# Kernel tuning notes

Measured on AMD Instinct MI355X. Metric: run time of the kernel, lower is better.

Reference implementation:

```python
import jax, jax.numpy as jnp
import numpy as np

B, N = 1, 1024
C_S, C_Z, N_HEAD, C_HEAD = 384, 128, 16, 24
HC = N_HEAD * C_HEAD


def _ln(x, eps=1e-5):
    m = jnp.mean(x, axis=-1, keepdims=True)
    v = jnp.var(x, axis=-1, keepdims=True)
    return (x - m) / jnp.sqrt(v + eps)


def setup_inputs() -> dict:
    key = jax.random.key(0)
    ks = jax.random.split(key, 24)
    w = lambda k, shp: (jax.random.normal(k, shp, jnp.float32) * 0.02)
    return {
        "a_i": jax.random.normal(ks[0], (B, N, C_S), jnp.float32),
        "s_i": jax.random.normal(ks[1], (B, N, C_S), jnp.float32),
        "z_ij": jax.random.normal(ks[2], (B, N, N, C_Z), jnp.float32),
        # AdaLN params
        "adaln_lns_w": jnp.ones((C_S,), jnp.float32),      # layer_norm_s weight (no bias)
        "adaln_ws": w(ks[3], (C_S, C_S)),                   # linear_s weight
        "adaln_bs": jnp.zeros((C_S,), jnp.float32),         # linear_s bias
        "adaln_wns": w(ks[4], (C_S, C_S)),                  # linear_no_bias_s
        # attention projections
        "wq": w(ks[5], (C_S, HC)),
        "bq": jnp.zeros((HC,), jnp.float32),
        "wk": w(ks[6], (C_S, HC)),
        "wv": w(ks[7], (C_S, HC)),
        # pair bias
        "lnb_w": jnp.ones((C_Z,), jnp.float32),
        "lnb_b": jnp.zeros((C_Z,), jnp.float32),
        "wb": w(ks[8], (C_Z, N_HEAD)),
        # gate + output
        "wg": w(ks[9], (C_S, HC)),
        "wo": w(ks[10], (HC, C_S)),
        # final conditioning gate (bias init -2.0 per module)
        "ws": w(ks[11], (C_S, C_S)),
        "bs": jnp.full((C_S,), -2.0, jnp.float32),
    }


def reference(a_i, s_i, z_ij, adaln_lns_w, adaln_ws, adaln_bs, adaln_wns,
              wq, bq, wk, wv, lnb_w, lnb_b, wb, wg, wo, ws, bs):
    b, n, _ = a_i.shape
    H, D = N_HEAD, C_HEAD
    # AdaLN: a <- sigmoid(Lin(s)) * LN(a) + Lin_nb(s)
    a = _ln(a_i)
    s = _ln(s_i) * adaln_lns_w
    a = jax.nn.sigmoid(s @ adaln_ws + adaln_bs) * a + s @ adaln_wns
    # QKV projections -> [b, i, h, d]
    q = (a @ wq + bq).reshape(b, n, H, D)
    k = (a @ wk).reshape(b, n, H, D)
    v = (a @ wv).reshape(b, n, H, D)
    # pair bias [b, h, i, j]
    bias = jnp.einsum('bijc,ch->bhij', _ln(z_ij) * lnb_w + lnb_b, wb)
    # gate [b, i, h, d]
    g = jax.nn.sigmoid(a @ wg).reshape(b, n, H, D)
    logits = jnp.einsum('bihd,bjhd->bhij', q, k) / jnp.sqrt(jnp.float32(D)) + bias
    A = jax.nn.softmax(logits, axis=-1)
    o = jnp.einsum('bhij,bjhd->bihd', A, v) * g
    o = o.reshape(b, n, H * D) @ wo
    # final gate uses raw s_i
    return jax.nn.sigmoid(s_i @ ws + bs) * o
```

## Files before the change

kernel.cpp:

```cpp
#include <hip/hip_runtime.h>
#include <hip/hip_bf16.h>
#include <math.h>

#define N_SEQ 1024
#define CS 384
#define CZ 128
#define NH 16
#define CH 24

typedef float  floatx4 __attribute__((ext_vector_type(4)));
typedef short  shortx8 __attribute__((ext_vector_type(8)));
typedef unsigned int uintx4 __attribute__((ext_vector_type(4)));

__device__ __forceinline__ unsigned short f2bf(float f){
  union { float fv; unsigned u; } c; c.fv = f;
  unsigned u = c.u;
  return (unsigned short)((u + 0x7fffu + ((u >> 16) & 1u)) >> 16);
}
__device__ __forceinline__ float bf2f(unsigned short s){
  union { unsigned u; float fv; } c; c.u = ((unsigned)s) << 16; return c.fv;
}
__device__ __forceinline__ float bf_lo(unsigned u){
  union { unsigned uu; float f; } c; c.uu = u << 16; return c.f;
}
__device__ __forceinline__ float bf_hi(unsigned u){
  union { unsigned uu; float f; } c; c.uu = u & 0xffff0000u; return c.f;
}
__device__ __forceinline__ float sigmoidf_(float x){ return 1.f / (1.f + __expf(-x)); }

__global__ __launch_bounds__(128) void ln_kernel(
    const float* __restrict__ a_i, const float* __restrict__ s_i,
    const float* __restrict__ lns_w,
    float* __restrict__ a_ln, float* __restrict__ s_ln)
{
  int i = blockIdx.x;
  int t = threadIdx.x;
  float av[3], sv[3];
  float sa = 0.f, qa = 0.f, ss = 0.f, qs = 0.f;
  #pragma unroll
  for (int e = 0; e < 3; ++e){
    int c = t + 128*e;
    float a = a_i[(size_t)i*CS + c];
    float s = s_i[(size_t)i*CS + c];
    av[e] = a; sv[e] = s;
    sa += a; qa += a*a; ss += s; qs += s*s;
  }
  #pragma unroll
  for (int off = 1; off < 64; off <<= 1){
    sa += __shfl_xor(sa, off);
    qa += __shfl_xor(qa, off);
    ss += __shfl_xor(ss, off);
    qs += __shfl_xor(qs, off);
  }
  __shared__ float red[2][4];
  if ((t & 63) == 0){
    int w = t >> 6;
    red[w][0] = sa; red[w][1] = qa; red[w][2] = ss; red[w][3] = qs;
  }
  __syncthreads();
  const float inv = 1.f / CS;
  float Sa = red[0][0] + red[1][0];
  float Qa = red[0][1] + red[1][1];
  float Ss = red[0][2] + red[1][2];
  float Qs = red[0][3] + red[1][3];
  float ma = Sa*inv, va = Qa*inv - ma*ma, ra = rsqrtf(va + 1e-5f);
  float ms = Ss*inv, vs = Qs*inv - ms*ms, rs = rsqrtf(vs + 1e-5f);
  #pragma unroll
  for (int e = 0; e < 3; ++e){
    int c = t + 128*e;
    a_ln[(size_t)i*CS + c] = (av[e] - ma) * ra;
    s_ln[(size_t)i*CS + c] = (sv[e] - ms) * rs * lns_w[c];
  }
}

__global__ __launch_bounds__(384) void gemm_kernel(
    const float* __restrict__ X, const float* __restrict__ W1,
    const float* __restrict__ B1, const float* __restrict__ W2,
    const float* __restrict__ extra,
    float* __restrict__ OUT1, float* __restrict__ OUT2, int mode)
{
  int r0 = blockIdx.x * 4;
  int t  = threadIdx.x;
  int ct = t % 96;
  int rg = t / 96;
  int c0 = ct * 4;
  __shared__ float xl[4][CS];
  #pragma unroll
  for (int rr = 0; rr < 4; ++rr)
    xl[rr][t] = X[(size_t)(r0+rr)*CS + t];
  __syncthreads();
  float acc1[4] = {0.f,0.f,0.f,0.f};
  float acc2[4] = {0.f,0.f,0.f,0.f};
  if (mode <= 2){
    for (int k = 0; k < CS; k += 4){
      floatx4 s4 = *(const floatx4*)&xl[rg][k];
      #pragma unroll
      for (int kk = 0; kk < 4; ++kk){
        floatx4 w1 = *(const floatx4*)&W1[(size_t)(k+kk)*CS + c0];
        floatx4 w2 = *(const floatx4*)&W2[(size_t)(k+kk)*CS + c0];
        #pragma unroll
        for (int cc = 0; cc < 4; ++cc){
          acc1[cc] += s4[kk] * w1[cc];
          acc2[cc] += s4[kk] * w2[cc];
        }
      }
    }
  } else {
    for (int k = 0; k < CS; k += 4){
      floatx4 s4 = *(const floatx4*)&xl[rg][k];
      #pragma unroll
      for (int kk = 0; kk < 4; ++kk){
        floatx4 w1 = *(const floatx4*)&W1[(size_t)(k+kk)*CS + c0];
        #pragma unroll
        for (int cc = 0; cc < 4; ++cc)
          acc1[cc] += s4[kk] * w1[cc];
      }
    }
  }
  int r = r0 + rg;
  size_t ob = (size_t)r * CS + c0;
  if (mode == 0){
    #pragma unroll
    for (int cc = 0; cc < 4; ++cc)
      OUT1[ob+cc] = sigmoidf_(acc1[cc] + B1[c0+cc]) * extra[ob+cc] + acc2[cc];
  } else if (mode == 1){
    #pragma unroll
    for (int cc = 0; cc < 4; ++cc){
      OUT1[ob+cc] = acc1[cc] + B1[c0+cc];
      OUT2[ob+cc] = acc2[cc];
    }
  } else if (mode == 2){
    #pragma unroll
    for (int cc = 0; cc < 4; ++cc){
      OUT1[ob+cc] = acc1[cc];
      OUT2[ob+cc] = sigmoidf_(acc2[cc]);
    }
  } else if (mode == 3){
    #pragma unroll
    for (int cc = 0; cc < 4; ++cc)
      OUT1[ob+cc] = acc1[cc];
  } else {
    #pragma unroll
    for (int cc = 0; cc < 4; ++cc)
      OUT1[ob+cc] = sigmoidf_(acc1[cc] + B1[c0+cc]) * extra[ob+cc];
  }
}

__global__ __launch_bounds__(256) void bias_kernel(
    const float* __restrict__ z, const float* __restrict__ lnb_w,
    const float* __restrict__ lnb_b, const float* __restrict__ wb,
    unsigned short* __restrict__ bias)
{
  int i    = blockIdx.x >> 4;
  int j0   = (blockIdx.x & 15) * 64;
  int wave = threadIdx.x >> 6;
  int lane = threadIdx.x & 63;
  int m    = lane & 15;
  int q    = lane >> 4;
  int jbase = j0 + wave * 16;

  shortx8 bfrag[4];
  float sumw = 0.f, sumb = 0.f;
  #pragma unroll
  for (int s = 0; s < 4; ++s){
    #pragma unroll
    for (int jj = 0; jj < 8; ++jj){
      int c = q*8 + jj + 32*s;
      float lw = lnb_w[c];
      float lb = lnb_b[c];
      float w  = wb[c*NH + m];
      bfrag[s][jj] = (short)f2bf(lw * w);
      sumw += lw * w;
      sumb += lb * w;
    }
  }
  sumw += __shfl_xor(sumw, 16); sumw += __shfl_xor(sumw, 32);
  sumb += __shfl_xor(sumb, 16); sumb += __shfl_xor(sumb, 32);

  const float* zrow = z + ((size_t)i * N_SEQ + (size_t)(jbase + m)) * CZ;
  floatx4 acc = {0.f, 0.f, 0.f, 0.f};
  float sum = 0.f, sq = 0.f;
  #pragma unroll
  for (int s = 0; s < 4; ++s){
    floatx4 z0 = *(const floatx4*)(zrow + q*8 + 32*s);
    floatx4 z1 = *(const floatx4*)(zrow + q*8 + 32*s + 4);
    shortx8 af;
    #pragma unroll
    for (int e = 0; e < 4; ++e){
      sum += z0[e]; sq += z0[e]*z0[e];
      sum += z1[e]; sq += z1[e]*z1[e];
      af[e]   = (short)f2bf(z0[e]);
      af[e+4] = (short)f2bf(z1[e]);
    }
    acc = __builtin_amdgcn_mfma_f32_16x16x32_bf16(af, bfrag[s], acc, 0, 0, 0);
  }
  sum += __shfl_xor(sum, 16); sum += __shfl_xor(sum, 32);
  sq  += __shfl_xor(sq , 16); sq  += __shfl_xor(sq , 32);
  float mean = sum * (1.f/CZ);
  float var  = sq  * (1.f/CZ) - mean*mean;
  float rstd = rsqrtf(var + 1e-5f);

  __shared__ float ob[NH][65];
  #pragma unroll
  for (int r = 0; r < 4; ++r){
    int row = q*4 + r;
    float mr = __shfl(mean, row);
    float rr = __shfl(rstd, row);
    ob[m][wave*16 + row] = rr * (acc[r] - mr * sumw) + sumb;
  }
  __syncthreads();
  size_t base = (size_t)i * N_SEQ + j0;
  #pragma unroll
  for (int rep = 0; rep < 4; ++rep){
    int idx = threadIdx.x + rep*256;
    int hh = idx >> 6;
    int jj = idx & 63;
    bias[(size_t)hh * ((size_t)N_SEQ*N_SEQ) + base + jj] = f2bf(ob[hh][jj]);
  }
}

#define TJ 128
#define KROW 20
__global__ __launch_bounds__(256) void attn_kernel(
    const float* __restrict__ qq, const float* __restrict__ kk,
    const float* __restrict__ vv, const float* __restrict__ gg,
    const unsigned short* __restrict__ bias, float* __restrict__ att)
{
  int h  = blockIdx.x & 15;
  int i0 = (blockIdx.x >> 4) * 16;
  int il = threadIdx.x & 15;
  int jg = threadIdx.x >> 4;

  __shared__ unsigned int smem[TJ*KROW*2];

  float qr[24];
  {
    const float* qs = qq + (size_t)(i0+il)*CS + h*CH;
    #pragma unroll
    for (int e = 0; e < 6; ++e){
      floatx4 t4 = *(const floatx4*)(qs + 4*e);
      qr[4*e] = t4[0]; qr[4*e+1] = t4[1]; qr[4*e+2] = t4[2]; qr[4*e+3] = t4[3];
    }
  }
  const float scale = 0.20412414523193154f;
  float lrun = 0.f;
  float o[24];
  #pragma unroll
  for (int d = 0; d < 24; ++d) o[d] = 0.f;

  for (int jt = 0; jt < 8; ++jt){
    __syncthreads();
    {
      int row  = threadIdx.x >> 1;
      int half = threadIdx.x & 1;
      const float* ks = kk + (size_t)(jt*TJ + row)*CS + h*CH + half*12;
      const float* vs = vv + (size_t)(jt*TJ + row)*CS + h*CH + half*12;
      unsigned int* kd = smem + row*KROW + half*6;
      unsigned int* vd = smem + TJ*KROW + row*KROW + half*6;
      #pragma unroll
      for (int e = 0; e < 6; ++e){
        kd[e] = (unsigned)f2bf(ks[2*e]) | ((unsigned)f2bf(ks[2*e+1]) << 16);
        vd[e] = (unsigned)f2bf(vs[2*e]) | ((unsigned)f2bf(vs[2*e+1]) << 16);
      }
    }
    __syncthreads();
    const unsigned short* bptr = bias + (size_t)h*((size_t)N_SEQ*N_SEQ)
                               + (size_t)(i0+il)*N_SEQ + jt*TJ;
    #pragma unroll
    for (int tt = 0; tt < 8; ++tt){
      int jl = jg + 16*tt;
      uintx4 k0 = *(const uintx4*)&smem[jl*KROW];
      uintx4 k1 = *(const uintx4*)&smem[jl*KROW + 4];
      uintx4 k2 = *(const uintx4*)&smem[jl*KROW + 8];
      float dot = 0.f;
      #pragma unroll
      for (int e = 0; e < 4; ++e){
        dot += bf_lo(k0[e])*qr[2*e]      + bf_hi(k0[e])*qr[2*e+1];
        dot += bf_lo(k1[e])*qr[8+2*e]    + bf_hi(k1[e])*qr[8+2*e+1];
        dot += bf_lo(k2[e])*qr[16+2*e]   + bf_hi(k2[e])*qr[16+2*e+1];
      }
      float p = __expf(dot * scale + bf2f(bptr[jl]));
      lrun += p;
      uintx4 v0 = *(const uintx4*)&smem[TJ*KROW + jl*KROW];
      uintx4 v1 = *(const uintx4*)&smem[TJ*KROW + jl*KROW + 4];
      uintx4 v2 = *(const uintx4*)&smem[TJ*KROW + jl*KROW + 8];
      #pragma unroll
      for (int e = 0; e < 4; ++e){
        o[2*e]      += p * bf_lo(v0[e]);  o[2*e+1]    += p * bf_hi(v0[e]);
        o[8+2*e]    += p * bf_lo(v1[e]);  o[8+2*e+1]  += p * bf_hi(v1[e]);
        o[16+2*e]   += p * bf_lo(v2[e]);  o[16+2*e+1] += p * bf_hi(v2[e]);
      }
    }
  }
  __syncthreads();
  #pragma unroll
  for (int d = 0; d < 24; ++d){
    o[d] += __shfl_xor(o[d], 16);
    o[d] += __shfl_xor(o[d], 32);
  }
  lrun += __shfl_xor(lrun, 16);
  lrun += __shfl_xor(lrun, 32);
  float* mgf = (float*)smem;
  int lane = threadIdx.x & 63;
  int w    = threadIdx.x >> 6;
  if (lane < 16){
    float* slot = mgf + (w*16 + lane)*25;
    slot[0] = lrun;
    #pragma unroll
    for (int d = 0; d < 24; ++d) slot[1+d] = o[d];
  }
  __syncthreads();
  if (threadIdx.x < 16){
    int ii = threadIdx.x;
    float L = 0.f, O[24];
    #pragma unroll
    for (int d = 0; d < 24; ++d) O[d] = 0.f;
    for (int w2 = 0; w2 < 4; ++w2){
      const float* slot = mgf + (w2*16 + ii)*25;
      L += slot[0];
      #pragma unroll
      for (int d = 0; d < 24; ++d) O[d] += slot[1+d];
    }
    const float* gs = gg + (size_t)(i0+ii)*CS + h*CH;
    float* os = att + (size_t)(i0+ii)*CS + h*CH;
    float invL = 1.f / L;
    #pragma unroll
    for (int d = 0; d < 24; ++d) os[d] = O[d] * invL * gs[d];
  }
}

extern "C" void kernel_launch(void* const* d_in, const int* in_sizes, int n_in,
                              void* d_out, int out_size, void* d_ws, size_t ws_size,
                              hipStream_t stream) {
  const float* a_i     = (const float*)d_in[0];
  const float* s_i     = (const float*)d_in[1];
  const float* z_ij    = (const float*)d_in[2];
  const float* lns_w   = (const float*)d_in[3];
  const float* ada_ws  = (const float*)d_in[4];
  const float* ada_bs  = (const float*)d_in[5];
  const float* ada_wns = (const float*)d_in[6];
  const float* wq      = (const float*)d_in[7];
  const float* bq      = (const float*)d_in[8];
  const float* wk      = (const float*)d_in[9];
  const float* wv      = (const float*)d_in[10];
  const float* lnb_w   = (const float*)d_in[11];
  const float* lnb_b   = (const float*)d_in[12];
  const float* wb      = (const float*)d_in[13];
  const float* wg      = (const float*)d_in[14];
  const float* wo      = (const float*)d_in[15];
  const float* wsm     = (const float*)d_in[16];
  const float* bsv     = (const float*)d_in[17];

  const size_t RC = (size_t)N_SEQ * CS;
  float* wsf  = (float*)d_ws;
  float* s_ln = wsf;
  float* a_ln = wsf + RC;
  float* a    = wsf + 2*RC;
  float* qv   = wsf + 3*RC;
  float* kv   = wsf + 4*RC;
  float* vvp  = wsf + 5*RC;
  float* gv   = wsf + 6*RC;
  float* attb = wsf + 7*RC;
  float* tmp  = wsf + 8*RC;
  unsigned short* biasw = (unsigned short*)(wsf + 9*RC);

  ln_kernel<<<N_SEQ, 128, 0, stream>>>(a_i, s_i, lns_w, a_ln, s_ln);
  gemm_kernel<<<N_SEQ/4, 384, 0, stream>>>(s_ln, ada_ws, ada_bs, ada_wns, a_ln, a, nullptr, 0);
  gemm_kernel<<<N_SEQ/4, 384, 0, stream>>>(a, wq, bq, wk, nullptr, qv, kv, 1);
  gemm_kernel<<<N_SEQ/4, 384, 0, stream>>>(a, wv, nullptr, wg, nullptr, vvp, gv, 2);
  bias_kernel<<<N_SEQ*16, 256, 0, stream>>>(z_ij, lnb_w, lnb_b, wb, biasw);
  attn_kernel<<<N_SEQ, 256, 0, stream>>>(qv, kv, vvp, gv, biasw, attb);
  gemm_kernel<<<N_SEQ/4, 384, 0, stream>>>(attb, wo, nullptr, nullptr, nullptr, tmp, nullptr, 3);
  gemm_kernel<<<N_SEQ/4, 384, 0, stream>>>(s_i, wsm, bsv, nullptr, tmp, (float*)d_out, nullptr, 4);
}
```

Baseline: 1.171 ms.

## Overlap pair-bias computation with LN and projection GEMMs via horizontal kernel fusion

The standalone bias kernel is split into chunks of 3072, 6656 and 6656 work units. These run as extra blocks inside the LN, AdaLN and QKVG GEMM kernels, so the memory-bound z_ij streaming overlaps with the small latency-bound GEMMs. The Q/K/V/G projections are merged into one kernel that reads the activations once, and the output projection is fused with the final sigmoid gate. This removes launches and intermediate buffers, but mixes block types with different launch bounds and shared-memory use in the same grid.

```diff
diff --git a/kernel.cpp b/kernel.cpp
--- a/kernel.cpp
+++ b/kernel.cpp
@@ -7,6 +7,7 @@
 #define CZ 128
 #define NH 16
 #define CH 24
+#define HC 384
 
 typedef float  floatx4 __attribute__((ext_vector_type(4)));
 typedef short  shortx8 __attribute__((ext_vector_type(8)));
@@ -28,20 +29,106 @@
 }
 __device__ __forceinline__ float sigmoidf_(float x){ return 1.f / (1.f + __expf(-x)); }
 
-__global__ __launch_bounds__(128) void ln_kernel(
+__device__ __forceinline__ void bias_unit(int u, int tid, int nthr,
+    const float* __restrict__ z, const float* __restrict__ lnb_w,
+    const float* __restrict__ lnb_b, const float* __restrict__ wb,
+    unsigned short* __restrict__ bias, float (*ob)[65])
+{
+  int i    = u >> 4;
+  int j0   = (u & 15) * 64;
+  int wave = tid >> 6;
+  int lane = tid & 63;
+
+  if (wave < 4){
+    int m = lane & 15;
+    int q = lane >> 4;
+    int jbase = j0 + wave * 16;
+
+    shortx8 bfrag[4];
+    float sumw = 0.f, sumb = 0.f;
+    #pragma unroll
+    for (int s = 0; s < 4; ++s){
+      #pragma unroll
+      for (int jj = 0; jj < 8; ++jj){
+        int c = q*8 + jj + 32*s;
+        float lw = lnb_w[c];
+        float lb = lnb_b[c];
+        float w  = wb[c*NH + m];
+        bfrag[s][jj] = (short)f2bf(lw * w);
+        sumw += lw * w;
+        sumb += lb * w;
+      }
+    }
+    sumw += __shfl_xor(sumw, 16); sumw += __shfl_xor(sumw, 32);
+    sumb += __shfl_xor(sumb, 16); sumb += __shfl_xor(sumb, 32);
+
+    const float* zrow = z + ((size_t)i * N_SEQ + (size_t)(jbase + m)) * CZ;
+    floatx4 acc = {0.f, 0.f, 0.f, 0.f};
+    float sum = 0.f, sq = 0.f;
+    #pragma unroll
+    for (int s = 0; s < 4; ++s){
+      floatx4 z0 = *(const floatx4*)(zrow + q*8 + 32*s);
+      floatx4 z1 = *(const floatx4*)(zrow + q*8 + 32*s + 4);
+      shortx8 af;
+      #pragma unroll
+      for (int e = 0; e < 4; ++e){
+        sum += z0[e]; sq += z0[e]*z0[e];
+        sum += z1[e]; sq += z1[e]*z1[e];
+        af[e]   = (short)f2bf(z0[e]);
+        af[e+4] = (short)f2bf(z1[e]);
+      }
+      acc = __builtin_amdgcn_mfma_f32_16x16x32_bf16(af, bfrag[s], acc, 0, 0, 0);
+    }
+    sum += __shfl_xor(sum, 16); sum += __shfl_xor(sum, 32);
+    sq  += __shfl_xor(sq , 16); sq  += __shfl_xor(sq , 32);
+    float mean = sum * (1.f/CZ);
+    float var  = sq  * (1.f/CZ) - mean*mean;
+    float rstd = rsqrtf(var + 1e-5f);
+
+    #pragma unroll
+    for (int r = 0; r < 4; ++r){
+      int row = q*4 + r;
+      float mr = __shfl(mean, row);
+      float rr = __shfl(rstd, row);
+      ob[m][wave*16 + row] = rr * (acc[r] - mr * sumw) + sumb;
+    }
+  }
+  __syncthreads();
+  size_t base = (size_t)i * N_SEQ + j0;
+  for (int idx = tid; idx < NH*64; idx += nthr){
+    int hh = idx >> 6;
+    int jj = idx & 63;
+    bias[(size_t)hh * ((size_t)N_SEQ*N_SEQ) + base + jj] = f2bf(ob[hh][jj]);
+  }
+}
+
+#define LN_BLOCKS 512
+#define NB1 3072
+__global__ __launch_bounds__(256) void ln_bias_kernel(
     const float* __restrict__ a_i, const float* __restrict__ s_i,
     const float* __restrict__ lns_w,
-    float* __restrict__ a_ln, float* __restrict__ s_ln)
-{
-  int i = blockIdx.x;
-  int t = threadIdx.x;
+    float* __restrict__ a_ln, float* __restrict__ s_ln,
+    const float* __restrict__ z, const float* __restrict__ lnb_w,
+    const float* __restrict__ lnb_b, const float* __restrict__ wb,
+    unsigned short* __restrict__ biasw)
+{
+  __shared__ float ob[NH][65];
+  if (blockIdx.x >= LN_BLOCKS){
+    bias_unit(blockIdx.x - LN_BLOCKS, threadIdx.x, 256, z, lnb_w, lnb_b, wb, biasw, ob);
+    return;
+  }
+  float* red = &ob[0][0];
+  int t    = threadIdx.x;
+  int half = t >> 7;
+  int tl   = t & 127;
+  int row  = blockIdx.x*2 + half;
   float av[3], sv[3];
   float sa = 0.f, qa = 0.f, ss = 0.f, qs = 0.f;
   #pragma unroll
   for (int e = 0; e < 3; ++e){
-    int c = t + 128*e;
-    float a = a_i[(size_t)i*CS + c];
-    float s = s_i[(size_t)i*CS + c];
+    int c = tl + 128*e;
+    float a = a_i[(size_t)row*CS + c];
+    float s = s_i[(size_t)row*CS + c];
     av[e] = a; sv[e] = s;
     sa += a; qa += a*a; ss += s; qs += s*s;
   }
@@ -52,170 +139,127 @@
     ss += __shfl_xor(ss, off);
     qs += __shfl_xor(qs, off);
   }
-  __shared__ float red[2][4];
   if ((t & 63) == 0){
     int w = t >> 6;
-    red[w][0] = sa; red[w][1] = qa; red[w][2] = ss; red[w][3] = qs;
+    red[w*4+0] = sa; red[w*4+1] = qa; red[w*4+2] = ss; red[w*4+3] = qs;
   }
   __syncthreads();
   const float inv = 1.f / CS;
-  float Sa = red[0][0] + red[1][0];
-  float Qa = red[0][1] + red[1][1];
-  float Ss = red[0][2] + red[1][2];
-  float Qs = red[0][3] + red[1][3];
+  int wb0 = half*2;
+  float Sa = red[wb0*4+0] + red[(wb0+1)*4+0];
+  float Qa = red[wb0*4+1] + red[(wb0+1)*4+1];
+  float Ss = red[wb0*4+2] + red[(wb0+1)*4+2];
+  float Qs = red[wb0*4+3] + red[(wb0+1)*4+3];
   float ma = Sa*inv, va = Qa*inv - ma*ma, ra = rsqrtf(va + 1e-5f);
   float ms = Ss*inv, vs = Qs*inv - ms*ms, rs = rsqrtf(vs + 1e-5f);
   #pragma unroll
   for (int e = 0; e < 3; ++e){
-    int c = t + 128*e;
-    a_ln[(size_t)i*CS + c] = (av[e] - ma) * ra;
-    s_ln[(size_t)i*CS + c] = (sv[e] - ms) * rs * lns_w[c];
-  }
-}
-
-__global__ __launch_bounds__(384) void gemm_kernel(
+    int c = tl + 128*e;
+    a_ln[(size_t)row*CS + c] = (av[e] - ma) * ra;
+    s_ln[(size_t)row*CS + c] = (sv[e] - ms) * rs * lns_w[c];
+  }
+}
+
+#define NB2 6656
+__global__ __launch_bounds__(384) void adaln_bias_kernel(
     const float* __restrict__ X, const float* __restrict__ W1,
     const float* __restrict__ B1, const float* __restrict__ W2,
-    const float* __restrict__ extra,
-    float* __restrict__ OUT1, float* __restrict__ OUT2, int mode)
-{
+    const float* __restrict__ extra, float* __restrict__ OUT,
+    const float* __restrict__ z, const float* __restrict__ lnb_w,
+    const float* __restrict__ lnb_b, const float* __restrict__ wb,
+    unsigned short* __restrict__ biasw)
+{
+  __shared__ float xl[4][CS];
+  if (blockIdx.x >= 256){
+    float (*ob)[65] = reinterpret_cast<float(*)[65]>(&xl[0][0]);
+    bias_unit(NB1 + (blockIdx.x - 256), threadIdx.x, 384, z, lnb_w, lnb_b, wb, biasw, ob);
+    return;
+  }
   int r0 = blockIdx.x * 4;
   int t  = threadIdx.x;
   int ct = t % 96;
   int rg = t / 96;
   int c0 = ct * 4;
-  __shared__ float xl[4][CS];
   #pragma unroll
   for (int rr = 0; rr < 4; ++rr)
     xl[rr][t] = X[(size_t)(r0+rr)*CS + t];
   __syncthreads();
   float acc1[4] = {0.f,0.f,0.f,0.f};
   float acc2[4] = {0.f,0.f,0.f,0.f};
-  if (mode <= 2){
-    for (int k = 0; k < CS; k += 4){
-      floatx4 s4 = *(const floatx4*)&xl[rg][k];
-      #pragma unroll
-      for (int kk = 0; kk < 4; ++kk){
-        floatx4 w1 = *(const floatx4*)&W1[(size_t)(k+kk)*CS + c0];
-        floatx4 w2 = *(const floatx4*)&W2[(size_t)(k+kk)*CS + c0];
-        #pragma unroll
-        for (int cc = 0; cc < 4; ++cc){
-          acc1[cc] += s4[kk] * w1[cc];
-          acc2[cc] += s4[kk] * w2[cc];
-        }
-      }
-    }
-  } else {
-    for (int k = 0; k < CS; k += 4){
-      floatx4 s4 = *(const floatx4*)&xl[rg][k];
-      #pragma unroll
-      for (int kk = 0; kk < 4; ++kk){
-        floatx4 w1 = *(const floatx4*)&W1[(size_t)(k+kk)*CS + c0];
-        #pragma unroll
-        for (int cc = 0; cc < 4; ++cc)
-          acc1[cc] += s4[kk] * w1[cc];
-      }
-    }
-  }
-  int r = r0 + rg;
-  size_t ob = (size_t)r * CS + c0;
-  if (mode == 0){
-    #pragma unroll
-    for (int cc = 0; cc < 4; ++cc)
-      OUT1[ob+cc] = sigmoidf_(acc1[cc] + B1[c0+cc]) * extra[ob+cc] + acc2[cc];
-  } else if (mode == 1){
-    #pragma unroll
-    for (int cc = 0; cc < 4; ++cc){
-      OUT1[ob+cc] = acc1[cc] + B1[c0+cc];
-      OUT2[ob+cc] = acc2[cc];
-    }
-  } else if (mode == 2){
-    #pragma unroll
-    for (int cc = 0; cc < 4; ++cc){
-      OUT1[ob+cc] = acc1[cc];
-      OUT2[ob+cc] = sigmoidf_(acc2[cc]);
-    }
-  } else if (mode == 3){
-    #pragma unroll
-    for (int cc = 0; cc < 4; ++cc)
-      OUT1[ob+cc] = acc1[cc];
-  } else {
-    #pragma unroll
-    for (int cc = 0; cc < 4; ++cc)
-      OUT1[ob+cc] = sigmoidf_(acc1[cc] + B1[c0+cc]) * extra[ob+cc];
-  }
-}
-
-__global__ __launch_bounds__(256) void bias_kernel(
+  for (int k = 0; k < CS; k += 4){
+    floatx4 s4 = *(const floatx4*)&xl[rg][k];
+    #pragma unroll
+    for (int kk = 0; kk < 4; ++kk){
+      floatx4 w1 = *(const floatx4*)&W1[(size_t)(k+kk)*CS + c0];
+      floatx4 w2 = *(const floatx4*)&W2[(size_t)(k+kk)*CS + c0];
+      #pragma unroll
+      for (int cc = 0; cc < 4; ++cc){
+        acc1[cc] += s4[kk] * w1[cc];
+        acc2[cc] += s4[kk] * w2[cc];
+      }
+    }
+  }
+  size_t obk = (size_t)(r0+rg) * CS + c0;
+  #pragma unroll
+  for (int cc = 0; cc < 4; ++cc)
+    OUT[obk+cc] = sigmoidf_(acc1[cc] + B1[c0+cc]) * extra[obk+cc] + acc2[cc];
+}
+
+#define NB3 6656
+__global__ __launch_bounds__(384) void qkvg_bias_kernel(
+    const float* __restrict__ X,
+    const float* __restrict__ wq, const float* __restrict__ bq,
+    const float* __restrict__ wk, const float* __restrict__ wv,
+    const float* __restrict__ wg,
+    float* __restrict__ qo, float* __restrict__ ko,
+    float* __restrict__ vo, float* __restrict__ go,
     const float* __restrict__ z, const float* __restrict__ lnb_w,
     const float* __restrict__ lnb_b, const float* __restrict__ wb,
-    unsigned short* __restrict__ bias)
-{
-  int i    = blockIdx.x >> 4;
-  int j0   = (blockIdx.x & 15) * 64;
-  int wave = threadIdx.x >> 6;
-  int lane = threadIdx.x & 63;
-  int m    = lane & 15;
-  int q    = lane >> 4;
-  int jbase = j0 + wave * 16;
-
-  shortx8 bfrag[4];
-  float sumw = 0.f, sumb = 0.f;
-  #pragma unroll
-  for (int s = 0; s < 4; ++s){
-    #pragma unroll
-    for (int jj = 0; jj < 8; ++jj){
-      int c = q*8 + jj + 32*s;
-      float lw = lnb_w[c];
-      float lb = lnb_b[c];
-      float w  = wb[c*NH + m];
-      bfrag[s][jj] = (short)f2bf(lw * w);
-      sumw += lw * w;
-      sumb += lb * w;
-    }
-  }
-  sumw += __shfl_xor(sumw, 16); sumw += __shfl_xor(sumw, 32);
-  sumb += __shfl_xor(sumb, 16); sumb += __shfl_xor(sumb, 32);
-
-  const float* zrow = z + ((size_t)i * N_SEQ + (size_t)(jbase + m)) * CZ;
-  floatx4 acc = {0.f, 0.f, 0.f, 0.f};
-  float sum = 0.f, sq = 0.f;
-  #pragma unroll
-  for (int s = 0; s < 4; ++s){
-    floatx4 z0 = *(const floatx4*)(zrow + q*8 + 32*s);
-    floatx4 z1 = *(const floatx4*)(zrow + q*8 + 32*s + 4);
-    shortx8 af;
-    #pragma unroll
-    for (int e = 0; e < 4; ++e){
-      sum += z0[e]; sq += z0[e]*z0[e];
-      sum += z1[e]; sq += z1[e]*z1[e];
-      af[e]   = (short)f2bf(z0[e]);
-      af[e+4] = (short)f2bf(z1[e]);
-    }
-    acc = __builtin_amdgcn_mfma_f32_16x16x32_bf16(af, bfrag[s], acc, 0, 0, 0);
-  }
-  sum += __shfl_xor(sum, 16); sum += __shfl_xor(sum, 32);
-  sq  += __shfl_xor(sq , 16); sq  += __shfl_xor(sq , 32);
-  float mean = sum * (1.f/CZ);
-  float var  = sq  * (1.f/CZ) - mean*mean;
-  float rstd = rsqrtf(var + 1e-5f);
-
-  __shared__ float ob[NH][65];
-  #pragma unroll
-  for (int r = 0; r < 4; ++r){
-    int row = q*4 + r;
-    float mr = __shfl(mean, row);
-    float rr = __shfl(rstd, row);
-    ob[m][wave*16 + row] = rr * (acc[r] - mr * sumw) + sumb;
-  }
-  __syncthreads();
-  size_t base = (size_t)i * N_SEQ + j0;
-  #pragma unroll
-  for (int rep = 0; rep < 4; ++rep){
-    int idx = threadIdx.x + rep*256;
-    int hh = idx >> 6;
-    int jj = idx & 63;
-    bias[(size_t)hh * ((size_t)N_SEQ*N_SEQ) + base + jj] = f2bf(ob[hh][jj]);
+    unsigned short* __restrict__ biasw)
+{
+  __shared__ float xl[4][CS];
+  if (blockIdx.x >= 256){
+    float (*ob)[65] = reinterpret_cast<float(*)[65]>(&xl[0][0]);
+    bias_unit(NB1 + NB2 + (blockIdx.x - 256), threadIdx.x, 384, z, lnb_w, lnb_b, wb, biasw, ob);
+    return;
+  }
+  int r0 = blockIdx.x * 4;
+  int t  = threadIdx.x;
+  int ct = t % 96;
+  int rg = t / 96;
+  int c0 = ct * 4;
+  #pragma unroll
+  for (int rr = 0; rr < 4; ++rr)
+    xl[rr][t] = X[(size_t)(r0+rr)*CS + t];
+  __syncthreads();
+  float aq[4] = {0.f,0.f,0.f,0.f};
+  float ak[4] = {0.f,0.f,0.f,0.f};
+  float av4[4] = {0.f,0.f,0.f,0.f};
+  float ag[4] = {0.f,0.f,0.f,0.f};
+  for (int k = 0; k < CS; k += 4){
+    floatx4 s4 = *(const floatx4*)&xl[rg][k];
+    #pragma unroll
+    for (int kk = 0; kk < 4; ++kk){
+      floatx4 wq4 = *(const floatx4*)&wq[(size_t)(k+kk)*HC + c0];
+      floatx4 wk4 = *(const floatx4*)&wk[(size_t)(k+kk)*HC + c0];
+      floatx4 wv4 = *(const floatx4*)&wv[(size_t)(k+kk)*HC + c0];
+      floatx4 wg4 = *(const floatx4*)&wg[(size_t)(k+kk)*HC + c0];
+      #pragma unroll
+      for (int cc = 0; cc < 4; ++cc){
+        aq[cc]  += s4[kk] * wq4[cc];
+        ak[cc]  += s4[kk] * wk4[cc];
+        av4[cc] += s4[kk] * wv4[cc];
+        ag[cc]  += s4[kk] * wg4[cc];
+      }
+    }
+  }
+  size_t obk = (size_t)(r0+rg) * HC + c0;
+  #pragma unroll
+  for (int cc = 0; cc < 4; ++cc){
+    qo[obk+cc] = aq[cc] + bq[c0+cc];
+    ko[obk+cc] = ak[cc];
+    vo[obk+cc] = av4[cc];
+    go[obk+cc] = sigmoidf_(ag[cc]);
   }
 }
 
@@ -327,6 +371,46 @@
     #pragma unroll
     for (int d = 0; d < 24; ++d) os[d] = O[d] * invL * gs[d];
   }
+}
+
+__global__ __launch_bounds__(384) void out_final_kernel(
+    const float* __restrict__ attb, const float* __restrict__ wo,
+    const float* __restrict__ s_i,  const float* __restrict__ wsm,
+    const float* __restrict__ bsv,  float* __restrict__ out)
+{
+  __shared__ float xo[4][CS];
+  __shared__ float xs[4][CS];
+  int r0 = blockIdx.x * 4;
+  int t  = threadIdx.x;
+  int ct = t % 96;
+  int rg = t / 96;
+  int c0 = ct * 4;
+  #pragma unroll
+  for (int rr = 0; rr < 4; ++rr){
+    xo[rr][t] = attb[(size_t)(r0+rr)*CS + t];
+    xs[rr][t] = s_i [(size_t)(r0+rr)*CS + t];
+  }
+  __syncthreads();
+  float ao[4] = {0.f,0.f,0.f,0.f};
+  float as[4] = {0.f,0.f,0.f,0.f};
+  for (int k = 0; k < CS; k += 4){
+    floatx4 o4 = *(const floatx4*)&xo[rg][k];
+    floatx4 s4 = *(const floatx4*)&xs[rg][k];
+    #pragma unroll
+    for (int kk = 0; kk < 4; ++kk){
+      floatx4 w1 = *(const floatx4*)&wo [(size_t)(k+kk)*CS + c0];
+      floatx4 w2 = *(const floatx4*)&wsm[(size_t)(k+kk)*CS + c0];
+      #pragma unroll
+      for (int cc = 0; cc < 4; ++cc){
+        ao[cc] += o4[kk] * w1[cc];
+        as[cc] += s4[kk] * w2[cc];
+      }
+    }
+  }
+  size_t obk = (size_t)(r0+rg) * CS + c0;
+  #pragma unroll
+  for (int cc = 0; cc < 4; ++cc)
+    out[obk+cc] = sigmoidf_(as[cc] + bsv[c0+cc]) * ao[cc];
 }
 
 extern "C" void kernel_launch(void* const* d_in, const int* in_sizes, int n_in,
@@ -361,15 +445,14 @@
   float* vvp  = wsf + 5*RC;
   float* gv   = wsf + 6*RC;
   float* attb = wsf + 7*RC;
-  float* tmp  = wsf + 8*RC;
   unsigned short* biasw = (unsigned short*)(wsf + 9*RC);
 
-  ln_kernel<<<N_SEQ, 128, 0, stream>>>(a_i, s_i, lns_w, a_ln, s_ln);
-  gemm_kernel<<<N_SEQ/4, 384, 0, stream>>>(s_ln, ada_ws, ada_bs, ada_wns, a_ln, a, nullptr, 0);
-  gemm_kernel<<<N_SEQ/4, 384, 0, stream>>>(a, wq, bq, wk, nullptr, qv, kv, 1);
-  gemm_kernel<<<N_SEQ/4, 384, 0, stream>>>(a, wv, nullptr, wg, nullptr, vvp, gv, 2);
-  bias_kernel<<<N_SEQ*16, 256, 0, stream>>>(z_ij, lnb_w, lnb_b, wb, biasw);
+  ln_bias_kernel<<<LN_BLOCKS + NB1, 256, 0, stream>>>(
+      a_i, s_i, lns_w, a_ln, s_ln, z_ij, lnb_w, lnb_b, wb, biasw);
+  adaln_bias_kernel<<<256 + NB2, 384, 0, stream>>>(
+      s_ln, ada_ws, ada_bs, ada_wns, a_ln, a, z_ij, lnb_w, lnb_b, wb, biasw);
+  qkvg_bias_kernel<<<256 + NB3, 384, 0, stream>>>(
+      a, wq, bq, wk, wv, wg, qv, kv, vvp, gv, z_ij, lnb_w, lnb_b, wb, biasw);
   attn_kernel<<<N_SEQ, 256, 0, stream>>>(qv, kv, vvp, gv, biasw, attb);
-  gemm_kernel<<<N_SEQ/4, 384, 0, stream>>>(attb, wo, nullptr, nullptr, nullptr, tmp, nullptr, 3);
-  gemm_kernel<<<N_SEQ/4, 384, 0, stream>>>(s_i, wsm, bsv, nullptr, tmp, (float*)d_out, nullptr, 4);
-}
+  out_final_kernel<<<256, 384, 0, stream>>>(attb, wo, s_i, wsm, bsv, (float*)d_out);
+}
```

New measurement: 1.060 ms. 1.1x faster.
